# Kernel tuning notes

Measured on AMD Instinct MI355X. Metric: run time of the kernel, lower is better.

## Reference

```python
import jax, jax.numpy as jnp
import numpy as np

N_HEAD = 16
HEAD_SIZE = 64
N_EMBD = 1024
B, T = 4, 2048
THETA = 10000.0


def _rope_cos_sin(t_len, dim):
    # freqs: (dim//2,), angles: (T, dim//2)
    inv = 1.0 / (THETA ** (jnp.arange(0, dim, 2, dtype=jnp.float32) / dim))
    ang = jnp.arange(t_len, dtype=jnp.float32)[:, None] * inv[None, :]
    return jnp.cos(ang), jnp.sin(ang)


def _apply_rope(x, cos, sin):
    # x: (B, H, T, hs) -> complex-pair rotation over last dim
    xr = x.reshape(*x.shape[:-1], -1, 2)
    x0, x1 = xr[..., 0], xr[..., 1]
    c = cos[None, None, :, :]
    s = sin[None, None, :, :]
    o0 = x0 * c - x1 * s
    o1 = x0 * s + x1 * c
    return jnp.stack([o0, o1], axis=-1).reshape(x.shape)


def setup_inputs() -> dict:
    key = jax.random.key(0)
    ks = jax.random.split(key, 5)
    scale = 1.0 / np.sqrt(N_EMBD)
    return {
        "x": jax.random.normal(ks[0], (B, T, N_EMBD), dtype=jnp.float32),
        "Wq": jax.random.normal(ks[1], (N_EMBD, N_HEAD * HEAD_SIZE), dtype=jnp.float32) * scale,
        "Wk": jax.random.normal(ks[2], (N_EMBD, N_HEAD * HEAD_SIZE), dtype=jnp.float32) * scale,
        "Wv": jax.random.normal(ks[3], (N_EMBD, N_HEAD * HEAD_SIZE), dtype=jnp.float32) * scale,
        "Wp": jax.random.normal(ks[4], (N_HEAD * HEAD_SIZE, N_EMBD), dtype=jnp.float32) * scale,
        "bp": jnp.zeros((N_EMBD,), dtype=jnp.float32),
    }


def reference(x, Wq, Wk, Wv, Wp, bp):
    Bx, Tx, C = x.shape
    q = (x @ Wq).reshape(Bx, Tx, N_HEAD, HEAD_SIZE).transpose(0, 2, 1, 3)
    k = (x @ Wk).reshape(Bx, Tx, N_HEAD, HEAD_SIZE).transpose(0, 2, 1, 3)
    v = (x @ Wv).reshape(Bx, Tx, N_HEAD, HEAD_SIZE).transpose(0, 2, 1, 3)
    cos, sin = _rope_cos_sin(Tx, HEAD_SIZE)
    q = _apply_rope(q, cos, sin)
    k = _apply_rope(k, cos, sin)
    wei = jnp.einsum('bhqd,bhkd->bhqk', q, k) * (HEAD_SIZE ** -0.5)
    causal = jnp.tril(jnp.ones((Tx, Tx), dtype=bool))
    wei = jnp.where(causal[None, None, :, :], wei, -jnp.inf)
    wei = jax.nn.softmax(wei, axis=-1)
    out = jnp.einsum('bhqk,bhkd->bhqd', wei, v)
    out = out.transpose(0, 2, 1, 3).reshape(Bx, Tx, N_HEAD * HEAD_SIZE)
    return out @ Wp + bp
```

## Files before the change

### kernel.cpp

```cpp
#include <hip/hip_runtime.h>
#include <hip/hip_bf16.h>

#define NH 16
#define HS 64
#define CE 1024
#define BB 4
#define TT 2048

typedef __bf16 bf16;
typedef __bf16 v8bf __attribute__((ext_vector_type(8)));
typedef __bf16 v4bf __attribute__((ext_vector_type(4)));
typedef __bf16 v2bf __attribute__((ext_vector_type(2)));
typedef float v4f __attribute__((ext_vector_type(4)));
typedef float v16f __attribute__((ext_vector_type(16)));

#define GLD16(gp, lp)                                                              \
    __builtin_amdgcn_global_load_lds((const __attribute__((address_space(1))) void*)(gp), \
                                     (__attribute__((address_space(3))) void*)(lp), 16, 0, 0)

#if __has_builtin(__builtin_amdgcn_exp2f)
#define EXP2(x) __builtin_amdgcn_exp2f(x)
#else
#define EXP2(x) exp2f(x)
#endif

__global__ __launch_bounds__(256) void cast_x_kernel(const float* __restrict__ x,
                                                     bf16* __restrict__ xb) {
    int idx = (blockIdx.x * 256 + threadIdx.x) * 8;
    const float4* xp = (const float4*)(x + idx);
    float4 a = xp[0], b = xp[1];
    v8bf o;
    o[0] = (bf16)a.x; o[1] = (bf16)a.y; o[2] = (bf16)a.z; o[3] = (bf16)a.w;
    o[4] = (bf16)b.x; o[5] = (bf16)b.y; o[6] = (bf16)b.z; o[7] = (bf16)b.w;
    *(v8bf*)(xb + idx) = o;
}

__global__ __launch_bounds__(256) void transpose_w_kernel(const float* __restrict__ W0,
                                                          const float* __restrict__ W1,
                                                          const float* __restrict__ W2,
                                                          const float* __restrict__ W3,
                                                          bf16* __restrict__ dqkv,
                                                          bf16* __restrict__ dp) {
    __shared__ bf16 tile[64][66];
    int z = blockIdx.z;
    const float* W = (z == 0) ? W0 : (z == 1) ? W1 : (z == 2) ? W2 : W3;
    bf16* Wt = (z < 3) ? (dqkv + (size_t)z * 1024 * CE) : dp;
    int k0 = blockIdx.x * 64;
    int n0 = blockIdx.y * 64;
    int tx = threadIdx.x & 63;
    int ty = threadIdx.x >> 6;
    for (int s = 0; s < 16; s++) {
        int r = s * 4 + ty;
        tile[r][tx] = (bf16)W[(size_t)(k0 + r) * CE + n0 + tx];
    }
    __syncthreads();
    for (int s = 0; s < 16; s++) {
        int r = s * 4 + ty;
        Wt[(size_t)(n0 + r) * CE + k0 + tx] = tile[tx][r];
    }
}

template <int MODE>
__global__ __launch_bounds__(256) void gemm_bt(const bf16* __restrict__ A,
                                               const bf16* __restrict__ Bt,
                                               bf16* __restrict__ Qb_, bf16* __restrict__ Kb_,
                                               bf16* __restrict__ Vt_,
                                               float* __restrict__ Pout,
                                               const float* __restrict__ bias) {
    __shared__ __align__(16) bf16 As[128 * 64];
    __shared__ __align__(16) bf16 Bs[128 * 64];
    const int tid = threadIdx.x;
    const int lane = tid & 63, wave = tid >> 6;
    const int lane15 = lane & 15, quad = lane >> 4;
    const int wr = wave >> 1, wc = wave & 1;
    const int m0 = blockIdx.y * 128;
    const int n0 = blockIdx.x * 128;

    v4f acc[4][4] = {};

    const int cm = tid >> 3;
    const int ck = ((tid & 7) ^ (cm & 7)) * 8;
    const bf16* Ag = A + (size_t)(m0 + cm) * CE + ck;
    const bf16* Bg = Bt + (size_t)(n0 + cm) * CE + ck;
    bf16* aD = &As[wave * 512];
    bf16* bD = &Bs[wave * 512];

    for (int k0 = 0; k0 < CE; k0 += 64) {
        __syncthreads();
#pragma unroll
        for (int p = 0; p < 4; p++) GLD16(Ag + k0 + (size_t)(p * 32) * CE, aD + p * 2048);
#pragma unroll
        for (int p = 0; p < 4; p++) GLD16(Bg + k0 + (size_t)(p * 32) * CE, bD + p * 2048);
        __syncthreads();
#pragma unroll
        for (int kh = 0; kh < 2; kh++) {
            v8bf af[4], bfr[4];
            for (int i = 0; i < 4; i++) {
                int row = wr * 64 + i * 16 + lane15;
                af[i] = *(const v8bf*)(&As[row * 64 + (((kh * 4 + quad) ^ (lane15 & 7)) * 8)]);
            }
            for (int j = 0; j < 4; j++) {
                int row = wc * 64 + j * 16 + lane15;
                bfr[j] = *(const v8bf*)(&Bs[row * 64 + (((kh * 4 + quad) ^ (lane15 & 7)) * 8)]);
            }
            for (int i = 0; i < 4; i++)
                for (int j = 0; j < 4; j++)
                    acc[i][j] = __builtin_amdgcn_mfma_f32_16x16x32_bf16(af[i], bfr[j], acc[i][j], 0, 0, 0);
        }
    }

    for (int i = 0; i < 4; i++) {
        for (int j = 0; j < 4; j++) {
            int gmb = m0 + wr * 64 + i * 16 + quad * 4;
            int gn = n0 + wc * 64 + j * 16 + lane15;
            if (MODE == 1) {
                float bb = bias[gn];
                for (int r = 0; r < 4; r++)
                    Pout[(size_t)(gmb + r) * CE + gn] = acc[i][j][r] + bb;
            } else {
                int w = gn >> 10;
                int n = gn & 1023;
                int h = n >> 6, d = n & 63;
                if (w < 2) {
                    bf16* out = w ? Kb_ : Qb_;
                    for (int r = 0; r < 4; r++) {
                        int gm = gmb + r;
                        int b = gm >> 11, t = gm & 2047;
                        out[(((size_t)(b * NH + h)) * TT + t) * HS + d] = (bf16)acc[i][j][r];
                    }
                } else {
                    int b = gmb >> 11, t = gmb & 2047;
                    v4bf pack;
                    for (int r = 0; r < 4; r++) pack[r] = (bf16)acc[i][j][r];
                    *(v4bf*)(&Vt_[(((size_t)(b * NH + h)) * HS + d) * TT + t]) = pack;
                }
            }
        }
    }
}

__global__ __launch_bounds__(256) void rope_kernel(bf16* __restrict__ Qb, bf16* __restrict__ Kb) {
    unsigned idx = blockIdx.x * 256 + threadIdx.x;
    bool isK = blockIdx.y != 0;
    bf16* buf = isK ? Kb : Qb;
    int i = idx & 31;
    int t = (idx >> 5) & 2047;
    float inv = exp2f(-0.41524101186092034f * (float)i);
    float ang = (float)t * inv;
    float s, c;
    sincosf(ang, &s, &c);
    if (!isK) {
        const float QS = 0.18033688011112042f;
        s *= QS; c *= QS;
    }
    bf16* p = buf + (size_t)idx * 2;
    v2bf v = *(v2bf*)p;
    float x0 = (float)v[0], x1 = (float)v[1];
    v2bf o;
    o[0] = (bf16)(x0 * c - x1 * s);
    o[1] = (bf16)(x0 * s + x1 * c);
    *(v2bf*)p = o;
}

__global__ __launch_bounds__(256, 4) void attn_kernel(const bf16* __restrict__ Qb,
                                                      const bf16* __restrict__ Kb,
                                                      const bf16* __restrict__ Vt,
                                                      bf16* __restrict__ Ob) {
    __shared__ __align__(16) bf16 Ks[32 * 64];
    __shared__ __align__(16) bf16 Vs[64 * 32];
    const int tid = threadIdx.x, lane = tid & 63, wave = tid >> 6;
    const int lane31 = lane & 31, h = lane >> 5;
    const int bh = blockIdx.x & 63;
    const int base = (blockIdx.x >> 6) & 3;
    const int g = blockIdx.x >> 8;
    const int qb = (g == 0) ? base : (g == 1) ? 7 - base : (g == 2) ? 8 + base : 15 - base;
    const int q0 = qb * 128 + wave * 32;
    const bf16* Qp = Qb + (size_t)bh * TT * HS;
    const bf16* Kp = Kb + (size_t)bh * TT * HS;
    const bf16* Vp = Vt + (size_t)bh * HS * TT;

    v8bf qf[4];
    for (int m = 0; m < 4; m++)
        qf[m] = *(const v8bf*)(Qp + (q0 + lane31) * HS + m * 16 + h * 8);

    v16f o0 = {}, o1 = {};
    float m_i = -3.0e38f, l_i = 0.f;

    const int kr = tid >> 3, kc = tid & 7;
    const bf16* kg = Kp + kr * HS + ((kc ^ (kr & 7)) * 8);
    const int vd = tid >> 2, vc = tid & 3;
    const bf16* vg = Vp + (size_t)vd * TT + ((vc ^ (vd & 3)) * 8);
    bf16* ksDst = &Ks[wave * 512];
    bf16* vsDst = &Vs[wave * 512];

    const int kv_max = qb * 128 + 96;
    for (int kv0 = 0; kv0 <= kv_max; kv0 += 32) {
        __syncthreads();
        GLD16(kg + kv0 * HS, ksDst);
        GLD16(vg + kv0, vsDst);
        __syncthreads();
        if (kv0 > q0) continue;
        const bool diag = (kv0 == q0);

        v16f s = {};
        for (int m = 0; m < 4; m++) {
            v8bf af = *(const v8bf*)(&Ks[lane31 * 64 + (((m << 1) | h) ^ (lane31 & 7)) * 8]);
            s = __builtin_amdgcn_mfma_f32_32x32x16_bf16(af, qf[m], s, 0, 0, 0);
        }

        float p[16];
        for (int r = 0; r < 16; r++) {
            float v = s[r];
            if (diag) {
                int kvr = (r & 3) + 8 * (r >> 2) + 4 * h;
                v = (kvr <= lane31) ? v : -3.0e38f;
            }
            p[r] = v;
        }
        float t8[8];
        for (int r = 0; r < 8; r++) t8[r] = fmaxf(p[r], p[r + 8]);
        float mx = fmaxf(fmaxf(fmaxf(t8[0], t8[1]), fmaxf(t8[2], t8[3])),
                         fmaxf(fmaxf(t8[4], t8[5]), fmaxf(t8[6], t8[7])));
        mx = fmaxf(mx, __shfl_xor(mx, 32));
        bool anyUpd = __ballot(mx > m_i) != 0ull;
        float mn = fmaxf(m_i, mx);
        for (int r = 0; r < 16; r++) p[r] = EXP2(p[r] - mn);
        float a8[8];
        for (int r = 0; r < 8; r++) a8[r] = p[r] + p[r + 8];
        float rs = ((a8[0] + a8[1]) + (a8[2] + a8[3])) + ((a8[4] + a8[5]) + (a8[6] + a8[7]));
        rs += __shfl_xor(rs, 32);
        if (anyUpd) {
            float alpha = EXP2(m_i - mn);
            m_i = mn;
            l_i = l_i * alpha + rs;
            for (int r = 0; r < 16; r++) { o0[r] *= alpha; o1[r] *= alpha; }
        } else {
            l_i += rs;
        }

        union { v4bf v; unsigned long long u; } ch[4];
        for (int gg = 0; gg < 4; gg++)
            for (int rr = 0; rr < 4; rr++)
                ch[gg].v[rr] = (bf16)p[gg * 4 + rr];

        for (int t = 0; t < 2; t++) {
            unsigned long long mine0 = ch[2 * t].u, mine1 = ch[2 * t + 1].u;
            unsigned long long send = h ? mine0 : mine1;
            unsigned long long recv = __shfl_xor(send, 32);
            union { v8bf v; unsigned long long u[2]; } bfr;
            bfr.u[0] = h ? recv : mine0;
            bfr.u[1] = h ? mine1 : recv;
            int cidx = (((t << 1) | h) ^ (lane31 & 3)) * 8;
            v8bf va0 = *(const v8bf*)(&Vs[lane31 * 32 + cidx]);
            o0 = __builtin_amdgcn_mfma_f32_32x32x16_bf16(va0, bfr.v, o0, 0, 0, 0);
            v8bf va1 = *(const v8bf*)(&Vs[(32 + lane31) * 32 + cidx]);
            o1 = __builtin_amdgcn_mfma_f32_32x32x16_bf16(va1, bfr.v, o1, 0, 0, 0);
        }
    }

    const int b = bh >> 4, hh = bh & 15;
    const int q = q0 + lane31;
    float invl = 1.f / l_i;
    bf16* outRow = Ob + ((size_t)(b * TT + q)) * CE + hh * HS;
    for (int gg = 0; gg < 4; gg++) {
        v4bf w0, w1;
        for (int rr = 0; rr < 4; rr++) {
            w0[rr] = (bf16)(o0[gg * 4 + rr] * invl);
            w1[rr] = (bf16)(o1[gg * 4 + rr] * invl);
        }
        *(v4bf*)(outRow + gg * 8 + h * 4) = w0;
        *(v4bf*)(outRow + 32 + gg * 8 + h * 4) = w1;
    }
}

extern "C" void kernel_launch(void* const* d_in, const int* in_sizes, int n_in,
                              void* d_out, int out_size, void* d_ws, size_t ws_size,
                              hipStream_t stream) {
    const float* x  = (const float*)d_in[0];
    const float* Wq = (const float*)d_in[1];
    const float* Wk = (const float*)d_in[2];
    const float* Wv = (const float*)d_in[3];
    const float* Wp = (const float*)d_in[4];
    const float* bp = (const float*)d_in[5];
    char* ws = (char*)d_ws;
    const size_t MB = 1024 * 1024;
    bf16* Xb    = (bf16*)(ws);
    bf16* WqkvT = (bf16*)(ws + 16 * MB);
    bf16* WpT   = (bf16*)(ws + 22 * MB);
    bf16* Qb    = (bf16*)(ws + 24 * MB);
    bf16* Kb    = (bf16*)(ws + 40 * MB);
    bf16* Vt    = (bf16*)(ws + 56 * MB);
    bf16* Ob    = (bf16*)(ws + 72 * MB);

    cast_x_kernel<<<dim3(4096), dim3(256), 0, stream>>>(x, Xb);
    transpose_w_kernel<<<dim3(16, 16, 4), dim3(256), 0, stream>>>(Wq, Wk, Wv, Wp, WqkvT, WpT);

    gemm_bt<0><<<dim3(24, 64), dim3(256), 0, stream>>>(Xb, WqkvT, Qb, Kb, Vt, nullptr, nullptr);

    rope_kernel<<<dim3(16384, 2), dim3(256), 0, stream>>>(Qb, Kb);

    attn_kernel<<<dim3(1024), dim3(256), 0, stream>>>(Qb, Kb, Vt, Ob);

    gemm_bt<1><<<dim3(8, 64), dim3(256), 0, stream>>>(Ob, WpT, nullptr, nullptr, nullptr,
                                                      (float*)d_out, bp);
}
```

Before: 276.9 us.

## Fuse RoPE into QKV GEMM epilogue and make attention single-wave without LDS

RoPE is folded into the QKV projection epilogue. A small kernel precomputes cos/sin tables, and each output lane pairs with its neighbour via a shuffle, which removes the separate rope read-modify-write pass. The attention kernel becomes one wave per 32-query block, reading K and V straight from global memory instead of staging them through LDS with barriers, and blocks are scheduled heaviest-first. In exchange, K/V tiles are no longer shared across waves, so global/L2 traffic rises, and EXP2 now uses exp2f rather than the hardware builtin.

```diff
diff --git a/kernel.cpp b/kernel.cpp
--- a/kernel.cpp
+++ b/kernel.cpp
@@ -18,11 +18,7 @@
     __builtin_amdgcn_global_load_lds((const __attribute__((address_space(1))) void*)(gp), \
                                      (__attribute__((address_space(3))) void*)(lp), 16, 0, 0)
 
-#if __has_builtin(__builtin_amdgcn_exp2f)
-#define EXP2(x) __builtin_amdgcn_exp2f(x)
-#else
 #define EXP2(x) exp2f(x)
-#endif
 
 __global__ __launch_bounds__(256) void cast_x_kernel(const float* __restrict__ x,
                                                      bf16* __restrict__ xb) {
@@ -33,6 +29,19 @@
     o[0] = (bf16)a.x; o[1] = (bf16)a.y; o[2] = (bf16)a.z; o[3] = (bf16)a.w;
     o[4] = (bf16)b.x; o[5] = (bf16)b.y; o[6] = (bf16)b.z; o[7] = (bf16)b.w;
     *(v8bf*)(xb + idx) = o;
+}
+
+__global__ __launch_bounds__(256) void cs_kernel(float2* __restrict__ csQ,
+                                                 float2* __restrict__ csK) {
+    int idx = blockIdx.x * 256 + threadIdx.x;
+    int t = idx >> 5, i = idx & 31;
+    float inv = exp2f(-0.41524101186092034f * (float)i);
+    float ang = (float)t * inv;
+    float s, c;
+    sincosf(ang, &s, &c);
+    const float QS = 0.18033688011112042f;
+    csK[idx] = make_float2(c, s);
+    csQ[idx] = make_float2(c * QS, s * QS);
 }
 
 __global__ __launch_bounds__(256) void transpose_w_kernel(const float* __restrict__ W0,
@@ -66,7 +75,9 @@
                                                bf16* __restrict__ Qb_, bf16* __restrict__ Kb_,
                                                bf16* __restrict__ Vt_,
                                                float* __restrict__ Pout,
-                                               const float* __restrict__ bias) {
+                                               const float* __restrict__ bias,
+                                               const float2* __restrict__ csQ,
+                                               const float2* __restrict__ csK) {
     __shared__ __align__(16) bf16 As[128 * 64];
     __shared__ __align__(16) bf16 Bs[128 * 64];
     const int tid = threadIdx.x;
@@ -120,93 +131,61 @@
             } else {
                 int w = gn >> 10;
                 int n = gn & 1023;
-                int h = n >> 6, d = n & 63;
+                int hh = n >> 6, d = n & 63;
                 if (w < 2) {
                     bf16* out = w ? Kb_ : Qb_;
+                    const float2* csRow = (w ? csK : csQ) + (d >> 1);
                     for (int r = 0; r < 4; r++) {
                         int gm = gmb + r;
                         int b = gm >> 11, t = gm & 2047;
-                        out[(((size_t)(b * NH + h)) * TT + t) * HS + d] = (bf16)acc[i][j][r];
+                        float xv = acc[i][j][r];
+                        float pv = __shfl_xor(xv, 1);
+                        float2 cs = csRow[t * 32];
+                        float ov = (gn & 1) ? (pv * cs.y + xv * cs.x)
+                                            : (xv * cs.x - pv * cs.y);
+                        out[(((size_t)(b * NH + hh)) * TT + t) * HS + d] = (bf16)ov;
                     }
                 } else {
                     int b = gmb >> 11, t = gmb & 2047;
                     v4bf pack;
                     for (int r = 0; r < 4; r++) pack[r] = (bf16)acc[i][j][r];
-                    *(v4bf*)(&Vt_[(((size_t)(b * NH + h)) * HS + d) * TT + t]) = pack;
+                    *(v4bf*)(&Vt_[(((size_t)(b * NH + hh)) * HS + d) * TT + t]) = pack;
                 }
             }
         }
     }
 }
 
-__global__ __launch_bounds__(256) void rope_kernel(bf16* __restrict__ Qb, bf16* __restrict__ Kb) {
-    unsigned idx = blockIdx.x * 256 + threadIdx.x;
-    bool isK = blockIdx.y != 0;
-    bf16* buf = isK ? Kb : Qb;
-    int i = idx & 31;
-    int t = (idx >> 5) & 2047;
-    float inv = exp2f(-0.41524101186092034f * (float)i);
-    float ang = (float)t * inv;
-    float s, c;
-    sincosf(ang, &s, &c);
-    if (!isK) {
-        const float QS = 0.18033688011112042f;
-        s *= QS; c *= QS;
-    }
-    bf16* p = buf + (size_t)idx * 2;
-    v2bf v = *(v2bf*)p;
-    float x0 = (float)v[0], x1 = (float)v[1];
-    v2bf o;
-    o[0] = (bf16)(x0 * c - x1 * s);
-    o[1] = (bf16)(x0 * s + x1 * c);
-    *(v2bf*)p = o;
-}
-
-__global__ __launch_bounds__(256, 4) void attn_kernel(const bf16* __restrict__ Qb,
-                                                      const bf16* __restrict__ Kb,
-                                                      const bf16* __restrict__ Vt,
-                                                      bf16* __restrict__ Ob) {
-    __shared__ __align__(16) bf16 Ks[32 * 64];
-    __shared__ __align__(16) bf16 Vs[64 * 32];
-    const int tid = threadIdx.x, lane = tid & 63, wave = tid >> 6;
+__global__ __launch_bounds__(64) void attn_kernel(const bf16* __restrict__ Qb,
+                                                  const bf16* __restrict__ Kb,
+                                                  const bf16* __restrict__ Vt,
+                                                  bf16* __restrict__ Ob) {
+    const int lane = threadIdx.x;
     const int lane31 = lane & 31, h = lane >> 5;
-    const int bh = blockIdx.x & 63;
-    const int base = (blockIdx.x >> 6) & 3;
-    const int g = blockIdx.x >> 8;
-    const int qb = (g == 0) ? base : (g == 1) ? 7 - base : (g == 2) ? 8 + base : 15 - base;
-    const int q0 = qb * 128 + wave * 32;
+    const unsigned bid = blockIdx.x;
+    const unsigned si = bid >> 3;
+    const int bh = (int)(bid & 7) * 8 + (int)(si & 7);
+    const int qw = 63 - (int)(si >> 3);
+    const int q0 = qw * 32;
     const bf16* Qp = Qb + (size_t)bh * TT * HS;
     const bf16* Kp = Kb + (size_t)bh * TT * HS;
     const bf16* Vp = Vt + (size_t)bh * HS * TT;
 
     v8bf qf[4];
     for (int m = 0; m < 4; m++)
-        qf[m] = *(const v8bf*)(Qp + (q0 + lane31) * HS + m * 16 + h * 8);
+        qf[m] = *(const v8bf*)(Qp + (size_t)(q0 + lane31) * HS + m * 16 + h * 8);
 
     v16f o0 = {}, o1 = {};
     float m_i = -3.0e38f, l_i = 0.f;
 
-    const int kr = tid >> 3, kc = tid & 7;
-    const bf16* kg = Kp + kr * HS + ((kc ^ (kr & 7)) * 8);
-    const int vd = tid >> 2, vc = tid & 3;
-    const bf16* vg = Vp + (size_t)vd * TT + ((vc ^ (vd & 3)) * 8);
-    bf16* ksDst = &Ks[wave * 512];
-    bf16* vsDst = &Vs[wave * 512];
-
-    const int kv_max = qb * 128 + 96;
-    for (int kv0 = 0; kv0 <= kv_max; kv0 += 32) {
-        __syncthreads();
-        GLD16(kg + kv0 * HS, ksDst);
-        GLD16(vg + kv0, vsDst);
-        __syncthreads();
-        if (kv0 > q0) continue;
+    for (int kv0 = 0; kv0 <= q0; kv0 += 32) {
         const bool diag = (kv0 == q0);
 
+        const bf16* kRow = Kp + (size_t)(kv0 + lane31) * HS + h * 8;
         v16f s = {};
-        for (int m = 0; m < 4; m++) {
-            v8bf af = *(const v8bf*)(&Ks[lane31 * 64 + (((m << 1) | h) ^ (lane31 & 7)) * 8]);
-            s = __builtin_amdgcn_mfma_f32_32x32x16_bf16(af, qf[m], s, 0, 0, 0);
-        }
+        for (int m = 0; m < 4; m++)
+            s = __builtin_amdgcn_mfma_f32_32x32x16_bf16(*(const v8bf*)(kRow + m * 16), qf[m], s,
+                                                        0, 0, 0);
 
         float p[16];
         for (int r = 0; r < 16; r++) {
@@ -239,10 +218,12 @@
         }
 
         union { v4bf v; unsigned long long u; } ch[4];
-        for (int gg = 0; gg < 4; gg++)
+        for (int g = 0; g < 4; g++)
             for (int rr = 0; rr < 4; rr++)
-                ch[gg].v[rr] = (bf16)p[gg * 4 + rr];
-
+                ch[g].v[rr] = (bf16)p[g * 4 + rr];
+
+        const bf16* vRow0 = Vp + (size_t)lane31 * TT + kv0 + h * 8;
+        const bf16* vRow1 = Vp + (size_t)(lane31 + 32) * TT + kv0 + h * 8;
         for (int t = 0; t < 2; t++) {
             unsigned long long mine0 = ch[2 * t].u, mine1 = ch[2 * t + 1].u;
             unsigned long long send = h ? mine0 : mine1;
@@ -250,11 +231,10 @@
             union { v8bf v; unsigned long long u[2]; } bfr;
             bfr.u[0] = h ? recv : mine0;
             bfr.u[1] = h ? mine1 : recv;
-            int cidx = (((t << 1) | h) ^ (lane31 & 3)) * 8;
-            v8bf va0 = *(const v8bf*)(&Vs[lane31 * 32 + cidx]);
-            o0 = __builtin_amdgcn_mfma_f32_32x32x16_bf16(va0, bfr.v, o0, 0, 0, 0);
-            v8bf va1 = *(const v8bf*)(&Vs[(32 + lane31) * 32 + cidx]);
-            o1 = __builtin_amdgcn_mfma_f32_32x32x16_bf16(va1, bfr.v, o1, 0, 0, 0);
+            o0 = __builtin_amdgcn_mfma_f32_32x32x16_bf16(*(const v8bf*)(vRow0 + t * 16), bfr.v,
+                                                         o0, 0, 0, 0);
+            o1 = __builtin_amdgcn_mfma_f32_32x32x16_bf16(*(const v8bf*)(vRow1 + t * 16), bfr.v,
+                                                         o1, 0, 0, 0);
         }
     }
 
@@ -262,14 +242,14 @@
     const int q = q0 + lane31;
     float invl = 1.f / l_i;
     bf16* outRow = Ob + ((size_t)(b * TT + q)) * CE + hh * HS;
-    for (int gg = 0; gg < 4; gg++) {
+    for (int g = 0; g < 4; g++) {
         v4bf w0, w1;
         for (int rr = 0; rr < 4; rr++) {
-            w0[rr] = (bf16)(o0[gg * 4 + rr] * invl);
-            w1[rr] = (bf16)(o1[gg * 4 + rr] * invl);
-        }
-        *(v4bf*)(outRow + gg * 8 + h * 4) = w0;
-        *(v4bf*)(outRow + 32 + gg * 8 + h * 4) = w1;
+            w0[rr] = (bf16)(o0[g * 4 + rr] * invl);
+            w1[rr] = (bf16)(o1[g * 4 + rr] * invl);
+        }
+        *(v4bf*)(outRow + g * 8 + h * 4) = w0;
+        *(v4bf*)(outRow + 32 + g * 8 + h * 4) = w1;
     }
 }
 
@@ -291,16 +271,18 @@
     bf16* Kb    = (bf16*)(ws + 40 * MB);
     bf16* Vt    = (bf16*)(ws + 56 * MB);
     bf16* Ob    = (bf16*)(ws + 72 * MB);
+    float2* csQ = (float2*)(ws + 72 * MB);
+    float2* csK = (float2*)(ws + 72 * MB + 512 * 1024);
 
     cast_x_kernel<<<dim3(4096), dim3(256), 0, stream>>>(x, Xb);
+    cs_kernel<<<dim3(256), dim3(256), 0, stream>>>(csQ, csK);
     transpose_w_kernel<<<dim3(16, 16, 4), dim3(256), 0, stream>>>(Wq, Wk, Wv, Wp, WqkvT, WpT);
 
-    gemm_bt<0><<<dim3(24, 64), dim3(256), 0, stream>>>(Xb, WqkvT, Qb, Kb, Vt, nullptr, nullptr);
-
-    rope_kernel<<<dim3(16384, 2), dim3(256), 0, stream>>>(Qb, Kb);
-
-    attn_kernel<<<dim3(1024), dim3(256), 0, stream>>>(Qb, Kb, Vt, Ob);
+    gemm_bt<0><<<dim3(24, 64), dim3(256), 0, stream>>>(Xb, WqkvT, Qb, Kb, Vt, nullptr, nullptr,
+                                                       csQ, csK);
+
+    attn_kernel<<<dim3(4096), dim3(64), 0, stream>>>(Qb, Kb, Vt, Ob);
 
     gemm_bt<1><<<dim3(8, 64), dim3(256), 0, stream>>>(Ob, WpT, nullptr, nullptr, nullptr,
-                                                      (float*)d_out, bp);
-}
+                                                      (float*)d_out, bp, nullptr, nullptr);
+}
```

New measurement: 332.5 us. 1.2x slower.
